# Kernel optimization log

Measured on AMD Instinct MI355X. Metric: run time of the kernel, lower is better.

## Reference

```python
import jax, jax.numpy as jnp
import numpy as np

B, N, C = 2, 2048, 1024
H = 16
D = C // H  # head_dim = 64
SCALE = D ** -0.5


def setup_inputs() -> dict:
    key = jax.random.key(0)
    k1, k2, k3, k4 = jax.random.split(key, 4)
    x = jax.random.normal(k1, (B, N, C), dtype=jnp.float32)
    # nn.Linear(in_dim, 3*out_dim, bias=False): store as [in, 3*out] for x @ W
    w_qkv = jax.random.normal(k2, (C, 3 * C), dtype=jnp.float32) * (C ** -0.5)
    w_proj = jax.random.normal(k3, (C, C), dtype=jnp.float32) * (C ** -0.5)
    b_proj = jax.random.normal(k4, (C,), dtype=jnp.float32) * 0.01
    return {"x": x, "w_qkv": w_qkv, "w_proj": w_proj, "b_proj": b_proj}


def reference(x, w_qkv, w_proj, b_proj):
    b, n, c = x.shape
    # QKV projection -> [3, B, H, N, D]
    qkv = (x @ w_qkv).reshape(b, n, 3, H, D).transpose(2, 0, 3, 1, 4)
    q, k, v = qkv[0], qkv[1], qkv[2]
    # scaled dot-product attention, full [B, H, N, N] scores as in original
    attn = jax.nn.softmax(jnp.einsum('bhqd,bhkd->bhqk', q * SCALE, k), axis=-1)
    out = jnp.einsum('bhqk,bhkd->bhqd', attn, v)  # [B, H, N, D]
    out = out.transpose(0, 2, 1, 3).reshape(b, n, c)
    return out @ w_proj + b_proj
```

## Files before the change

kernel.cpp:

```cpp
#include <hip/hip_runtime.h>

typedef unsigned short u16;
typedef float f32x4 __attribute__((ext_vector_type(4)));
typedef short bf16x8 __attribute__((ext_vector_type(8)));
typedef u16 u16x4 __attribute__((ext_vector_type(4)));
typedef u16 u16x8 __attribute__((ext_vector_type(8)));
typedef __bf16 bfr4 __attribute__((ext_vector_type(4)));

#define BB 2
#define NN 2048
#define CC 1024
#define HH 16
#define DD 64
#define MM (BB * NN)
#define NQKV (3 * CC)
#define QSCALE 0.18033688011112042f

#if __has_builtin(__builtin_amdgcn_exp2f)
#define EXP2(x) __builtin_amdgcn_exp2f(x)
#else
#define EXP2(x) exp2f(x)
#endif

__device__ __forceinline__ u16 f2bf(float f) {
    unsigned u = __float_as_uint(f);
    u += 0x7FFFu + ((u >> 16) & 1u);
    return (u16)(u >> 16);
}

__device__ __forceinline__ void ld_lds16(const u16* g, u16* l) {
    __builtin_amdgcn_global_load_lds(
        (const __attribute__((address_space(1))) unsigned int*)g,
        (__attribute__((address_space(3))) unsigned int*)l, 16, 0, 0);
}

__global__ __launch_bounds__(256) void k_tobf(const float* __restrict__ in,
                                              u16* __restrict__ out, int n) {
    int i = (blockIdx.x * 256 + threadIdx.x) * 8;
    if (i >= n) return;
    float4 a = *(const float4*)(in + i);
    float4 b = *(const float4*)(in + i + 4);
    u16x8 o;
    o[0] = f2bf(a.x); o[1] = f2bf(a.y); o[2] = f2bf(a.z); o[3] = f2bf(a.w);
    o[4] = f2bf(b.x); o[5] = f2bf(b.y); o[6] = f2bf(b.z); o[7] = f2bf(b.w);
    *(u16x8*)(out + i) = o;
}

__global__ __launch_bounds__(256) void k_tcast(const float* __restrict__ in,
                                               u16* __restrict__ out,
                                               int K, int Nn) {
    __shared__ float tile[32][33];
    int t = threadIdx.x, tx = t & 31, ty = t >> 5;
    int n0 = blockIdx.x * 32, k0 = blockIdx.y * 32;
#pragma unroll
    for (int r = 0; r < 32; r += 8)
        tile[ty + r][tx] = in[(size_t)(k0 + ty + r) * Nn + n0 + tx];
    __syncthreads();
#pragma unroll
    for (int r = 0; r < 32; r += 8)
        out[(size_t)(n0 + ty + r) * K + k0 + tx] = f2bf(tile[tx][ty + r]);
}

template <int MODE>
__global__ __launch_bounds__(256) void k_gemm(
    const u16* __restrict__ A, const u16* __restrict__ B,
    u16* __restrict__ Qb, u16* __restrict__ Kb, u16* __restrict__ Vb,
    const float* __restrict__ bias, float* __restrict__ Cout) {
    const int Kd = 1024;
    __shared__ __align__(16) u16 Ah[128][32];
    __shared__ __align__(16) u16 Bh[128][32];

    int t = threadIdx.x;
    int wave = t >> 6, lane = t & 63;
    int quad = lane >> 4, l16 = lane & 15;
    int wm = (wave >> 1) * 64, wn = (wave & 1) * 64;
    int m0 = blockIdx.y * 128, n0 = blockIdx.x * 128;

    int strow0 = wave * 16 + (lane >> 2);
    int stdst  = (lane & 3) * 8;
    int stsrc  = ((lane & 3) ^ ((lane >> 3) & 3)) * 8;
    int cfrag = (quad ^ ((l16 >> 1) & 3)) * 8;

    f32x4 acc[4][4];
#pragma unroll
    for (int i = 0; i < 4; i++)
#pragma unroll
        for (int j = 0; j < 4; j++) acc[i][j] = f32x4{0.f, 0.f, 0.f, 0.f};

    for (int k0 = 0; k0 < Kd; k0 += 32) {
        __syncthreads();
#pragma unroll
        for (int ii = 0; ii < 2; ii++) {
            int row = strow0 + ii * 64;
            ld_lds16(A + (size_t)(m0 + row) * Kd + k0 + stsrc, &Ah[row][stdst]);
            ld_lds16(B + (size_t)(n0 + row) * Kd + k0 + stsrc, &Bh[row][stdst]);
        }
        __syncthreads();

        bf16x8 af[4], bf[4];
#pragma unroll
        for (int i = 0; i < 4; i++) {
            af[i] = *(const bf16x8*)&Ah[wm + i * 16 + l16][cfrag];
            bf[i] = *(const bf16x8*)&Bh[wn + i * 16 + l16][cfrag];
        }
#pragma unroll
        for (int mi = 0; mi < 4; mi++)
#pragma unroll
            for (int ni = 0; ni < 4; ni++)
                acc[mi][ni] = __builtin_amdgcn_mfma_f32_16x16x32_bf16(
                    af[mi], bf[ni], acc[mi][ni], 0, 0, 0);
    }

#pragma unroll
    for (int mi = 0; mi < 4; mi++)
#pragma unroll
        for (int ni = 0; ni < 4; ni++)
#pragma unroll
            for (int r = 0; r < 4; r++) {
                int grow = m0 + wm + mi * 16 + quad * 4 + r;
                int gcol = n0 + wn + ni * 16 + l16;
                float v = acc[mi][ni][r];
                if (MODE == 0) {
                    int three = gcol >> 10, rem = gcol & 1023;
                    int h = rem >> 6, d = rem & 63;
                    int bb = grow >> 11, nn = grow & 2047;
                    if (three == 0) {
                        Qb[((size_t)(bb * HH + h) * NN + nn) * DD + d] = f2bf(v * QSCALE);
                    } else if (three == 1) {
                        Kb[((size_t)(bb * HH + h) * NN + nn) * DD + d] = f2bf(v);
                    } else {
                        Vb[((size_t)(bb * HH + h) * DD + d) * NN + nn] = f2bf(v);
                    }
                } else {
                    Cout[(size_t)grow * CC + gcol] = v + bias[gcol];
                }
            }
}

__global__ __launch_bounds__(256) void k_attn(const u16* __restrict__ Qb,
                                              const u16* __restrict__ Kb,
                                              const u16* __restrict__ VbT,
                                              u16* __restrict__ Ob) {
    __shared__ __align__(16) u16 Ks[64][64];
    __shared__ __align__(16) u16 Vs[64][64];
    __shared__ __align__(16) u16 Ps[4][32][72];

    int t = threadIdx.x, wave = t >> 6, lane = t & 63;
    int quad = lane >> 4, l16 = lane & 15;
    int bh = blockIdx.y, q0 = blockIdx.x * 128;
    const size_t kbase = (size_t)bh * NN * DD;
    const size_t vbase = (size_t)bh * DD * NN;

    bf16x8 qf[2][2];
#pragma unroll
    for (int qj = 0; qj < 2; qj++) {
        int qrow = q0 + wave * 32 + qj * 16 + l16;
        qf[qj][0] = *(const bf16x8*)&Qb[kbase + (size_t)qrow * DD + quad * 8];
        qf[qj][1] = *(const bf16x8*)&Qb[kbase + (size_t)qrow * DD + 32 + quad * 8];
    }

    f32x4 o[4][2];
#pragma unroll
    for (int i = 0; i < 4; i++)
#pragma unroll
        for (int j = 0; j < 2; j++) o[i][j] = f32x4{0.f, 0.f, 0.f, 0.f};
    float lrow[2] = {0.f, 0.f};

    int stgrp = lane & 7;
    int stsrc = (stgrp ^ (lane >> 3)) * 8;
    int strow0 = wave * 8 + (lane >> 3);
    int cf0 = (quad ^ (l16 & 7)) * 8;
    int cf1 = ((4 + quad) ^ (l16 & 7)) * 8;

    for (int c = 0; c < NN / 64; c++) {
        __syncthreads();
#pragma unroll
        for (int ii = 0; ii < 2; ii++) {
            int row = strow0 + ii * 32;
            ld_lds16(&Kb[kbase + (size_t)(c * 64 + row) * DD + stsrc], &Ks[row][stgrp * 8]);
            ld_lds16(&VbT[vbase + (size_t)row * NN + c * 64 + stsrc], &Vs[row][stgrp * 8]);
        }
        __syncthreads();

        bf16x8 kf[4][2];
#pragma unroll
        for (int kt = 0; kt < 4; kt++) {
            kf[kt][0] = *(const bf16x8*)&Ks[kt * 16 + l16][cf0];
            kf[kt][1] = *(const bf16x8*)&Ks[kt * 16 + l16][cf1];
        }

#pragma unroll
        for (int qj = 0; qj < 2; qj++) {
            f32x4 s[4];
#pragma unroll
            for (int kt = 0; kt < 4; kt++) {
                f32x4 z = f32x4{0.f, 0.f, 0.f, 0.f};
                z = __builtin_amdgcn_mfma_f32_16x16x32_bf16(kf[kt][0], qf[qj][0], z, 0, 0, 0);
                z = __builtin_amdgcn_mfma_f32_16x16x32_bf16(kf[kt][1], qf[qj][1], z, 0, 0, 0);
                s[kt] = z;
            }
            float sum = lrow[qj];
#pragma unroll
            for (int kt = 0; kt < 4; kt++) {
                bfr4 pk;
#pragma unroll
                for (int r = 0; r < 4; r++) {
                    float e = EXP2(s[kt][r]);
                    sum += e;
                    pk[r] = (__bf16)e;
                }
                *(bfr4*)&Ps[wave][qj * 16 + l16][kt * 16 + quad * 4] = pk;
            }
            lrow[qj] = sum;
        }
        __asm__ volatile("s_waitcnt lgkmcnt(0)" ::: "memory");
        bf16x8 pb[2][2];
#pragma unroll
        for (int qj = 0; qj < 2; qj++) {
            pb[qj][0] = *(const bf16x8*)&Ps[wave][qj * 16 + l16][quad * 8];
            pb[qj][1] = *(const bf16x8*)&Ps[wave][qj * 16 + l16][32 + quad * 8];
        }
#pragma unroll
        for (int dt = 0; dt < 4; dt++) {
            bf16x8 vf0 = *(const bf16x8*)&Vs[dt * 16 + l16][cf0];
            bf16x8 vf1 = *(const bf16x8*)&Vs[dt * 16 + l16][cf1];
#pragma unroll
            for (int qj = 0; qj < 2; qj++) {
                o[dt][qj] = __builtin_amdgcn_mfma_f32_16x16x32_bf16(vf0, pb[qj][0], o[dt][qj], 0, 0, 0);
                o[dt][qj] = __builtin_amdgcn_mfma_f32_16x16x32_bf16(vf1, pb[qj][1], o[dt][qj], 0, 0, 0);
            }
        }
    }

    int b = bh >> 4, h = bh & 15;
#pragma unroll
    for (int qj = 0; qj < 2; qj++) {
        float l = lrow[qj];
        l += __shfl_xor(l, 16, 64);
        l += __shfl_xor(l, 32, 64);
        float inv = 1.f / l;
        int grow = b * NN + q0 + wave * 32 + qj * 16 + l16;
#pragma unroll
        for (int dt = 0; dt < 4; dt++) {
            u16x4 hv;
#pragma unroll
            for (int r = 0; r < 4; r++) hv[r] = f2bf(o[dt][qj][r] * inv);
            int gcol = h * DD + dt * 16 + quad * 4;
            *(u16x4*)&Ob[(size_t)grow * CC + gcol] = hv;
        }
    }
}

extern "C" void kernel_launch(void* const* d_in, const int* in_sizes, int n_in,
                              void* d_out, int out_size, void* d_ws, size_t ws_size,
                              hipStream_t stream) {
    const float* x      = (const float*)d_in[0];
    const float* w_qkv  = (const float*)d_in[1];
    const float* w_proj = (const float*)d_in[2];
    const float* b_proj = (const float*)d_in[3];
    float* out = (float*)d_out;

    u16* p = (u16*)d_ws;
    u16* Xb = p; p += (size_t)MM * CC;
    u16* Wq = p; p += (size_t)NQKV * CC;
    u16* Wp = p; p += (size_t)CC * CC;
    u16* Qb = p; p += (size_t)MM * CC;
    u16* Kb = p; p += (size_t)MM * CC;
    u16* Vb = p; p += (size_t)MM * CC;
    u16* Ob = p; p += (size_t)MM * CC;

    k_tobf<<<(MM * CC) / (256 * 8), 256, 0, stream>>>(x, Xb, MM * CC);
    k_tcast<<<dim3(NQKV / 32, CC / 32), 256, 0, stream>>>(w_qkv, Wq, CC, NQKV);
    k_tcast<<<dim3(CC / 32, CC / 32), 256, 0, stream>>>(w_proj, Wp, CC, CC);
    k_gemm<0><<<dim3(NQKV / 128, MM / 128), 256, 0, stream>>>(
        Xb, Wq, Qb, Kb, Vb, nullptr, nullptr);
    k_attn<<<dim3(NN / 128, BB * HH), 256, 0, stream>>>(Qb, Kb, Vb, Ob);
    k_gemm<1><<<dim3(CC / 128, MM / 128), 256, 0, stream>>>(
        Ob, Wp, nullptr, nullptr, nullptr, b_proj, out);
}
```

Baseline: 200.2 us.

## Deepen GEMM K-tile to 64 and shrink attention query tile with MFMA row sums

The GEMM now stages a 64-wide K slice per iteration with an 8-group XOR swizzle, which halves the number of barrier pairs and issues two MFMAs per fragment pair. The attention kernel drops from 128 to 64 queries per block (16 per wave), doubling grid size for occupancy. It also replaces the scalar exp-sum and cross-lane shuffles with an MFMA against a vector of ones. The P scratch buffer is swizzled instead of padded. The trade-off is that K/V tiles are reloaded by twice as many blocks, and the row-sum is taken from bf16-rounded probabilities.

New measurement: 222.9 us. 11.3% more time.

```diff
diff --git a/kernel.cpp b/kernel.cpp
--- a/kernel.cpp
+++ b/kernel.cpp
@@ -67,8 +67,8 @@
     u16* __restrict__ Qb, u16* __restrict__ Kb, u16* __restrict__ Vb,
     const float* __restrict__ bias, float* __restrict__ Cout) {
     const int Kd = 1024;
-    __shared__ __align__(16) u16 Ah[128][32];
-    __shared__ __align__(16) u16 Bh[128][32];
+    __shared__ __align__(16) u16 Ah[128][64];
+    __shared__ __align__(16) u16 Bh[128][64];
 
     int t = threadIdx.x;
     int wave = t >> 6, lane = t & 63;
@@ -76,10 +76,11 @@
     int wm = (wave >> 1) * 64, wn = (wave & 1) * 64;
     int m0 = blockIdx.y * 128, n0 = blockIdx.x * 128;
 
-    int strow0 = wave * 16 + (lane >> 2);
-    int stdst  = (lane & 3) * 8;
-    int stsrc  = ((lane & 3) ^ ((lane >> 3) & 3)) * 8;
-    int cfrag = (quad ^ ((l16 >> 1) & 3)) * 8;
+    int stgrp  = lane & 7;
+    int strow0 = wave * 8 + (lane >> 3);
+    int stsrc  = (stgrp ^ (lane >> 3)) * 8;
+    int cf0 = (quad ^ (l16 & 7)) * 8;
+    int cf1 = ((4 + quad) ^ (l16 & 7)) * 8;
 
     f32x4 acc[4][4];
 #pragma unroll
@@ -87,28 +88,33 @@
 #pragma unroll
         for (int j = 0; j < 4; j++) acc[i][j] = f32x4{0.f, 0.f, 0.f, 0.f};
 
-    for (int k0 = 0; k0 < Kd; k0 += 32) {
-        __syncthreads();
-#pragma unroll
-        for (int ii = 0; ii < 2; ii++) {
-            int row = strow0 + ii * 64;
-            ld_lds16(A + (size_t)(m0 + row) * Kd + k0 + stsrc, &Ah[row][stdst]);
-            ld_lds16(B + (size_t)(n0 + row) * Kd + k0 + stsrc, &Bh[row][stdst]);
-        }
-        __syncthreads();
-
-        bf16x8 af[4], bf[4];
+    for (int k0 = 0; k0 < Kd; k0 += 64) {
+        __syncthreads();
+#pragma unroll
+        for (int ii = 0; ii < 4; ii++) {
+            int row = strow0 + ii * 32;
+            ld_lds16(A + (size_t)(m0 + row) * Kd + k0 + stsrc, &Ah[row][stgrp * 8]);
+            ld_lds16(B + (size_t)(n0 + row) * Kd + k0 + stsrc, &Bh[row][stgrp * 8]);
+        }
+        __syncthreads();
+
+        bf16x8 af0[4], af1[4], bf0[4], bf1[4];
 #pragma unroll
         for (int i = 0; i < 4; i++) {
-            af[i] = *(const bf16x8*)&Ah[wm + i * 16 + l16][cfrag];
-            bf[i] = *(const bf16x8*)&Bh[wn + i * 16 + l16][cfrag];
+            af0[i] = *(const bf16x8*)&Ah[wm + i * 16 + l16][cf0];
+            af1[i] = *(const bf16x8*)&Ah[wm + i * 16 + l16][cf1];
+            bf0[i] = *(const bf16x8*)&Bh[wn + i * 16 + l16][cf0];
+            bf1[i] = *(const bf16x8*)&Bh[wn + i * 16 + l16][cf1];
         }
 #pragma unroll
         for (int mi = 0; mi < 4; mi++)
 #pragma unroll
-            for (int ni = 0; ni < 4; ni++)
+            for (int ni = 0; ni < 4; ni++) {
                 acc[mi][ni] = __builtin_amdgcn_mfma_f32_16x16x32_bf16(
-                    af[mi], bf[ni], acc[mi][ni], 0, 0, 0);
+                    af0[mi], bf0[ni], acc[mi][ni], 0, 0, 0);
+                acc[mi][ni] = __builtin_amdgcn_mfma_f32_16x16x32_bf16(
+                    af1[mi], bf1[ni], acc[mi][ni], 0, 0, 0);
+            }
     }
 
 #pragma unroll
@@ -143,34 +149,33 @@
                                               u16* __restrict__ Ob) {
     __shared__ __align__(16) u16 Ks[64][64];
     __shared__ __align__(16) u16 Vs[64][64];
-    __shared__ __align__(16) u16 Ps[4][32][72];
+    __shared__ __align__(16) u16 Ps[4][16][64];
 
     int t = threadIdx.x, wave = t >> 6, lane = t & 63;
     int quad = lane >> 4, l16 = lane & 15;
-    int bh = blockIdx.y, q0 = blockIdx.x * 128;
+    int bh = blockIdx.y, q0 = blockIdx.x * 64;
     const size_t kbase = (size_t)bh * NN * DD;
     const size_t vbase = (size_t)bh * DD * NN;
 
-    bf16x8 qf[2][2];
-#pragma unroll
-    for (int qj = 0; qj < 2; qj++) {
-        int qrow = q0 + wave * 32 + qj * 16 + l16;
-        qf[qj][0] = *(const bf16x8*)&Qb[kbase + (size_t)qrow * DD + quad * 8];
-        qf[qj][1] = *(const bf16x8*)&Qb[kbase + (size_t)qrow * DD + 32 + quad * 8];
-    }
-
-    f32x4 o[4][2];
-#pragma unroll
-    for (int i = 0; i < 4; i++)
-#pragma unroll
-        for (int j = 0; j < 2; j++) o[i][j] = f32x4{0.f, 0.f, 0.f, 0.f};
-    float lrow[2] = {0.f, 0.f};
-
-    int stgrp = lane & 7;
-    int stsrc = (stgrp ^ (lane >> 3)) * 8;
+    int qrow = q0 + wave * 16 + l16;
+    bf16x8 qf0 = *(const bf16x8*)&Qb[kbase + (size_t)qrow * DD + quad * 8];
+    bf16x8 qf1 = *(const bf16x8*)&Qb[kbase + (size_t)qrow * DD + 32 + quad * 8];
+
+    bf16x8 ones;
+#pragma unroll
+    for (int j = 0; j < 8; j++) ones[j] = (short)0x3F80;
+
+    f32x4 o[4];
+    f32x4 accl = f32x4{0.f, 0.f, 0.f, 0.f};
+#pragma unroll
+    for (int i = 0; i < 4; i++) o[i] = f32x4{0.f, 0.f, 0.f, 0.f};
+
+    int stgrp  = lane & 7;
+    int stsrc  = (stgrp ^ (lane >> 3)) * 8;
     int strow0 = wave * 8 + (lane >> 3);
     int cf0 = (quad ^ (l16 & 7)) * 8;
     int cf1 = ((4 + quad) ^ (l16 & 7)) * 8;
+    int psw = (quad & 1) * 4;
 
     for (int c = 0; c < NN / 64; c++) {
         __syncthreads();
@@ -182,72 +187,51 @@
         }
         __syncthreads();
 
-        bf16x8 kf[4][2];
+        f32x4 s[4];
 #pragma unroll
         for (int kt = 0; kt < 4; kt++) {
-            kf[kt][0] = *(const bf16x8*)&Ks[kt * 16 + l16][cf0];
-            kf[kt][1] = *(const bf16x8*)&Ks[kt * 16 + l16][cf1];
-        }
-
-#pragma unroll
-        for (int qj = 0; qj < 2; qj++) {
-            f32x4 s[4];
-#pragma unroll
-            for (int kt = 0; kt < 4; kt++) {
-                f32x4 z = f32x4{0.f, 0.f, 0.f, 0.f};
-                z = __builtin_amdgcn_mfma_f32_16x16x32_bf16(kf[kt][0], qf[qj][0], z, 0, 0, 0);
-                z = __builtin_amdgcn_mfma_f32_16x16x32_bf16(kf[kt][1], qf[qj][1], z, 0, 0, 0);
-                s[kt] = z;
-            }
-            float sum = lrow[qj];
-#pragma unroll
-            for (int kt = 0; kt < 4; kt++) {
-                bfr4 pk;
-#pragma unroll
-                for (int r = 0; r < 4; r++) {
-                    float e = EXP2(s[kt][r]);
-                    sum += e;
-                    pk[r] = (__bf16)e;
-                }
-                *(bfr4*)&Ps[wave][qj * 16 + l16][kt * 16 + quad * 4] = pk;
-            }
-            lrow[qj] = sum;
+            bf16x8 kf0 = *(const bf16x8*)&Ks[kt * 16 + l16][cf0];
+            bf16x8 kf1 = *(const bf16x8*)&Ks[kt * 16 + l16][cf1];
+            f32x4 z = f32x4{0.f, 0.f, 0.f, 0.f};
+            z = __builtin_amdgcn_mfma_f32_16x16x32_bf16(kf0, qf0, z, 0, 0, 0);
+            z = __builtin_amdgcn_mfma_f32_16x16x32_bf16(kf1, qf1, z, 0, 0, 0);
+            s[kt] = z;
+        }
+
+#pragma unroll
+        for (int kt = 0; kt < 4; kt++) {
+            bfr4 pk;
+#pragma unroll
+            for (int r = 0; r < 4; r++) pk[r] = (__bf16)EXP2(s[kt][r]);
+            int og = 2 * kt + (quad >> 1);
+            *(bfr4*)&Ps[wave][l16][(og ^ (l16 & 7)) * 8 + psw] = pk;
         }
         __asm__ volatile("s_waitcnt lgkmcnt(0)" ::: "memory");
-        bf16x8 pb[2][2];
-#pragma unroll
-        for (int qj = 0; qj < 2; qj++) {
-            pb[qj][0] = *(const bf16x8*)&Ps[wave][qj * 16 + l16][quad * 8];
-            pb[qj][1] = *(const bf16x8*)&Ps[wave][qj * 16 + l16][32 + quad * 8];
-        }
+        bf16x8 pb0 = *(const bf16x8*)&Ps[wave][l16][cf0];
+        bf16x8 pb1 = *(const bf16x8*)&Ps[wave][l16][cf1];
+
+        accl = __builtin_amdgcn_mfma_f32_16x16x32_bf16(ones, pb0, accl, 0, 0, 0);
+        accl = __builtin_amdgcn_mfma_f32_16x16x32_bf16(ones, pb1, accl, 0, 0, 0);
+
 #pragma unroll
         for (int dt = 0; dt < 4; dt++) {
             bf16x8 vf0 = *(const bf16x8*)&Vs[dt * 16 + l16][cf0];
             bf16x8 vf1 = *(const bf16x8*)&Vs[dt * 16 + l16][cf1];
-#pragma unroll
-            for (int qj = 0; qj < 2; qj++) {
-                o[dt][qj] = __builtin_amdgcn_mfma_f32_16x16x32_bf16(vf0, pb[qj][0], o[dt][qj], 0, 0, 0);
-                o[dt][qj] = __builtin_amdgcn_mfma_f32_16x16x32_bf16(vf1, pb[qj][1], o[dt][qj], 0, 0, 0);
-            }
+            o[dt] = __builtin_amdgcn_mfma_f32_16x16x32_bf16(vf0, pb0, o[dt], 0, 0, 0);
+            o[dt] = __builtin_amdgcn_mfma_f32_16x16x32_bf16(vf1, pb1, o[dt], 0, 0, 0);
         }
     }
 
     int b = bh >> 4, h = bh & 15;
-#pragma unroll
-    for (int qj = 0; qj < 2; qj++) {
-        float l = lrow[qj];
-        l += __shfl_xor(l, 16, 64);
-        l += __shfl_xor(l, 32, 64);
-        float inv = 1.f / l;
-        int grow = b * NN + q0 + wave * 32 + qj * 16 + l16;
-#pragma unroll
-        for (int dt = 0; dt < 4; dt++) {
-            u16x4 hv;
-#pragma unroll
-            for (int r = 0; r < 4; r++) hv[r] = f2bf(o[dt][qj][r] * inv);
-            int gcol = h * DD + dt * 16 + quad * 4;
-            *(u16x4*)&Ob[(size_t)grow * CC + gcol] = hv;
-        }
+    float inv = 1.f / accl[0];
+    int grow = b * NN + q0 + wave * 16 + l16;
+#pragma unroll
+    for (int dt = 0; dt < 4; dt++) {
+        u16x4 hv;
+#pragma unroll
+        for (int r = 0; r < 4; r++) hv[r] = f2bf(o[dt][r] * inv);
+        int gcol = h * DD + dt * 16 + quad * 4;
+        *(u16x4*)&Ob[(size_t)grow * CC + gcol] = hv;
     }
 }
 
@@ -274,7 +258,7 @@
     k_tcast<<<dim3(CC / 32, CC / 32), 256, 0, stream>>>(w_proj, Wp, CC, CC);
     k_gemm<0><<<dim3(NQKV / 128, MM / 128), 256, 0, stream>>>(
         Xb, Wq, Qb, Kb, Vb, nullptr, nullptr);
-    k_attn<<<dim3(NN / 128, BB * HH), 256, 0, stream>>>(Qb, Kb, Vb, Ob);
+    k_attn<<<dim3(NN / 64, BB * HH), 256, 0, stream>>>(Qb, Kb, Vb, Ob);
     k_gemm<1><<<dim3(CC / 128, MM / 128), 256, 0, stream>>>(
         Ob, Wp, nullptr, nullptr, nullptr, b_proj, out);
 }
```

## Use two waves of 64 query rows each and compute row sums via MFMA

Applied to the files above, without the earlier changes.

The attention kernel now runs 128 threads (2 waves), each handling 64 query rows instead of 32, so every K/V fragment read from LDS feeds twice as many MFMAs. The softmax row sum is no longer built from scalar adds plus cross-lane shuffles; it is computed by an MFMA of the bf16 probabilities against a ones vector. The P tile in LDS gets an XOR swizzle so the P fragments can be read with the same conflict-avoiding pattern as K and V. The costs are higher register pressure, fewer waves to hide latency per block, and extra MFMA work for the row sums.

Result: slower. 214.2 us (+7.0%).

```diff
diff --git a/kernel.cpp b/kernel.cpp
--- a/kernel.cpp
+++ b/kernel.cpp
@@ -137,13 +137,13 @@
             }
 }
 
-__global__ __launch_bounds__(256) void k_attn(const u16* __restrict__ Qb,
+__global__ __launch_bounds__(128) void k_attn(const u16* __restrict__ Qb,
                                               const u16* __restrict__ Kb,
                                               const u16* __restrict__ VbT,
                                               u16* __restrict__ Ob) {
     __shared__ __align__(16) u16 Ks[64][64];
     __shared__ __align__(16) u16 Vs[64][64];
-    __shared__ __align__(16) u16 Ps[4][32][72];
+    __shared__ __align__(16) u16 Ps[2][64][64];
 
     int t = threadIdx.x, wave = t >> 6, lane = t & 63;
     int quad = lane >> 4, l16 = lane & 15;
@@ -151,32 +151,39 @@
     const size_t kbase = (size_t)bh * NN * DD;
     const size_t vbase = (size_t)bh * DD * NN;
 
-    bf16x8 qf[2][2];
-#pragma unroll
-    for (int qj = 0; qj < 2; qj++) {
-        int qrow = q0 + wave * 32 + qj * 16 + l16;
+    bf16x8 qf[4][2];
+#pragma unroll
+    for (int qj = 0; qj < 4; qj++) {
+        int qrow = q0 + wave * 64 + qj * 16 + l16;
         qf[qj][0] = *(const bf16x8*)&Qb[kbase + (size_t)qrow * DD + quad * 8];
         qf[qj][1] = *(const bf16x8*)&Qb[kbase + (size_t)qrow * DD + 32 + quad * 8];
     }
 
-    f32x4 o[4][2];
-#pragma unroll
-    for (int i = 0; i < 4; i++)
-#pragma unroll
-        for (int j = 0; j < 2; j++) o[i][j] = f32x4{0.f, 0.f, 0.f, 0.f};
-    float lrow[2] = {0.f, 0.f};
-
-    int stgrp = lane & 7;
-    int stsrc = (stgrp ^ (lane >> 3)) * 8;
+    bf16x8 ones;
+#pragma unroll
+    for (int j = 0; j < 8; j++) ones[j] = (short)0x3F80;
+
+    f32x4 o[4][4];
+    f32x4 accl[4];
+#pragma unroll
+    for (int i = 0; i < 4; i++) {
+        accl[i] = f32x4{0.f, 0.f, 0.f, 0.f};
+#pragma unroll
+        for (int j = 0; j < 4; j++) o[i][j] = f32x4{0.f, 0.f, 0.f, 0.f};
+    }
+
+    int stgrp  = lane & 7;
+    int stsrc  = (stgrp ^ (lane >> 3)) * 8;
     int strow0 = wave * 8 + (lane >> 3);
     int cf0 = (quad ^ (l16 & 7)) * 8;
     int cf1 = ((4 + quad) ^ (l16 & 7)) * 8;
+    int psw = (quad & 1) * 4;
 
     for (int c = 0; c < NN / 64; c++) {
         __syncthreads();
 #pragma unroll
-        for (int ii = 0; ii < 2; ii++) {
-            int row = strow0 + ii * 32;
+        for (int ii = 0; ii < 4; ii++) {
+            int row = strow0 + ii * 16;
             ld_lds16(&Kb[kbase + (size_t)(c * 64 + row) * DD + stsrc], &Ks[row][stgrp * 8]);
             ld_lds16(&VbT[vbase + (size_t)row * NN + c * 64 + stsrc], &Vs[row][stgrp * 8]);
         }
@@ -190,7 +197,7 @@
         }
 
 #pragma unroll
-        for (int qj = 0; qj < 2; qj++) {
+        for (int qj = 0; qj < 4; qj++) {
             f32x4 s[4];
 #pragma unroll
             for (int kt = 0; kt < 4; kt++) {
@@ -199,33 +206,31 @@
                 z = __builtin_amdgcn_mfma_f32_16x16x32_bf16(kf[kt][1], qf[qj][1], z, 0, 0, 0);
                 s[kt] = z;
             }
-            float sum = lrow[qj];
 #pragma unroll
             for (int kt = 0; kt < 4; kt++) {
                 bfr4 pk;
 #pragma unroll
-                for (int r = 0; r < 4; r++) {
-                    float e = EXP2(s[kt][r]);
-                    sum += e;
-                    pk[r] = (__bf16)e;
-                }
-                *(bfr4*)&Ps[wave][qj * 16 + l16][kt * 16 + quad * 4] = pk;
-            }
-            lrow[qj] = sum;
+                for (int r = 0; r < 4; r++) pk[r] = (__bf16)EXP2(s[kt][r]);
+                int og = 2 * kt + (quad >> 1);
+                *(bfr4*)&Ps[wave][qj * 16 + l16][(og ^ (l16 & 7)) * 8 + psw] = pk;
+            }
         }
         __asm__ volatile("s_waitcnt lgkmcnt(0)" ::: "memory");
-        bf16x8 pb[2][2];
-#pragma unroll
-        for (int qj = 0; qj < 2; qj++) {
-            pb[qj][0] = *(const bf16x8*)&Ps[wave][qj * 16 + l16][quad * 8];
-            pb[qj][1] = *(const bf16x8*)&Ps[wave][qj * 16 + l16][32 + quad * 8];
+
+        bf16x8 pb[4][2];
+#pragma unroll
+        for (int qj = 0; qj < 4; qj++) {
+            pb[qj][0] = *(const bf16x8*)&Ps[wave][qj * 16 + l16][cf0];
+            pb[qj][1] = *(const bf16x8*)&Ps[wave][qj * 16 + l16][cf1];
+            accl[qj] = __builtin_amdgcn_mfma_f32_16x16x32_bf16(ones, pb[qj][0], accl[qj], 0, 0, 0);
+            accl[qj] = __builtin_amdgcn_mfma_f32_16x16x32_bf16(ones, pb[qj][1], accl[qj], 0, 0, 0);
         }
 #pragma unroll
         for (int dt = 0; dt < 4; dt++) {
             bf16x8 vf0 = *(const bf16x8*)&Vs[dt * 16 + l16][cf0];
             bf16x8 vf1 = *(const bf16x8*)&Vs[dt * 16 + l16][cf1];
 #pragma unroll
-            for (int qj = 0; qj < 2; qj++) {
+            for (int qj = 0; qj < 4; qj++) {
                 o[dt][qj] = __builtin_amdgcn_mfma_f32_16x16x32_bf16(vf0, pb[qj][0], o[dt][qj], 0, 0, 0);
                 o[dt][qj] = __builtin_amdgcn_mfma_f32_16x16x32_bf16(vf1, pb[qj][1], o[dt][qj], 0, 0, 0);
             }
@@ -234,12 +239,9 @@
 
     int b = bh >> 4, h = bh & 15;
 #pragma unroll
-    for (int qj = 0; qj < 2; qj++) {
-        float l = lrow[qj];
-        l += __shfl_xor(l, 16, 64);
-        l += __shfl_xor(l, 32, 64);
-        float inv = 1.f / l;
-        int grow = b * NN + q0 + wave * 32 + qj * 16 + l16;
+    for (int qj = 0; qj < 4; qj++) {
+        float inv = 1.f / accl[qj][0];
+        int grow = b * NN + q0 + wave * 64 + qj * 16 + l16;
 #pragma unroll
         for (int dt = 0; dt < 4; dt++) {
             u16x4 hv;
@@ -274,7 +276,7 @@
     k_tcast<<<dim3(CC / 32, CC / 32), 256, 0, stream>>>(w_proj, Wp, CC, CC);
     k_gemm<0><<<dim3(NQKV / 128, MM / 128), 256, 0, stream>>>(
         Xb, Wq, Qb, Kb, Vb, nullptr, nullptr);
-    k_attn<<<dim3(NN / 128, BB * HH), 256, 0, stream>>>(Qb, Kb, Vb, Ob);
+    k_attn<<<dim3(NN / 128, BB * HH), 128, 0, stream>>>(Qb, Kb, Vb, Ob);
     k_gemm<1><<<dim3(CC / 128, MM / 128), 256, 0, stream>>>(
         Ob, Wp, nullptr, nullptr, nullptr, b_proj, out);
 }
```
